# Kernel optimization log

Hardware: AMD Instinct MI355X
Metric: run time of the kernel (lower is better)

Reference implementation:

```python
import jax, jax.numpy as jnp
import numpy as np

N_SRC = 50000
N_DST = 50000
E = 800000
SRC_DIM = 128
DST_DIM = 128
OUT_DIM = 128
HEADS = 4
D_HEAD = OUT_DIM // HEADS  # 32, concat=True


def setup_inputs() -> dict:
    key = jax.random.key(0)
    ks = jax.random.split(key, 10)
    x_src = jax.random.normal(ks[0], (N_SRC, SRC_DIM), dtype=jnp.float32)
    x_dst = jax.random.normal(ks[1], (N_DST, DST_DIM), dtype=jnp.float32)
    edge_src = jax.random.randint(ks[2], (E,), 0, N_SRC)
    edge_dst = jax.random.randint(ks[3], (E,), 0, N_DST)
    # parameters (torch Linear stored as [in, out] so y = x @ W)
    W_src = jax.random.normal(ks[4], (SRC_DIM, HEADS * D_HEAD), dtype=jnp.float32) / np.sqrt(SRC_DIM)
    W_dst = jax.random.normal(ks[5], (DST_DIM, HEADS * D_HEAD), dtype=jnp.float32) / np.sqrt(DST_DIM)
    att_src = jax.random.normal(ks[6], (1, HEADS, D_HEAD), dtype=jnp.float32) * 0.01
    att_dst = jax.random.normal(ks[7], (1, HEADS, D_HEAD), dtype=jnp.float32) * 0.01
    W_self = jax.random.normal(ks[8], (DST_DIM, HEADS * D_HEAD), dtype=jnp.float32) / np.sqrt(DST_DIM)
    b_self = jax.random.normal(ks[9], (HEADS * D_HEAD,), dtype=jnp.float32) * 0.01
    return {
        "x_src": x_src, "x_dst": x_dst,
        "edge_src": edge_src, "edge_dst": edge_dst, "num_dst": N_DST,
        "W_src": W_src, "W_dst": W_dst,
        "att_src": att_src, "att_dst": att_dst,
        "W_self": W_self, "b_self": b_self,
    }


def reference(x_src, x_dst, edge_src, edge_dst, num_dst,
              W_src, W_dst, att_src, att_dst, W_self, b_self):
    H, D = HEADS, D_HEAD
    src_feat = (x_src @ W_src).reshape(-1, H, D)   # [N_src, H, D]
    dst_feat = (x_dst @ W_dst).reshape(-1, H, D)   # [N_dst, H, D]

    src_edge = src_feat[edge_src]                   # [E, H, D] gather
    dst_edge = dst_feat[edge_dst]                   # [E, H, D] gather

    alpha_src = jnp.sum(src_edge * att_src, axis=-1)  # [E, H]
    alpha_dst = jnp.sum(dst_edge * att_dst, axis=-1)  # [E, H]
    alpha = jax.nn.leaky_relu(alpha_src + alpha_dst, negative_slope=0.2)

    # segment softmax over edges grouped by destination node
    a_max = jax.ops.segment_max(alpha, edge_dst, num_segments=num_dst)  # [N_dst, H]
    alpha = jnp.exp(alpha - a_max[edge_dst])
    a_sum = jax.ops.segment_sum(alpha, edge_dst, num_segments=num_dst)  # [N_dst, H]
    alpha = alpha / (a_sum[edge_dst] + 1e-16)

    msg = (src_edge * alpha[..., None]).reshape(-1, H * D)  # [E, H*D]
    agg = jax.ops.segment_sum(msg, edge_dst, num_segments=num_dst)  # [N_dst, H*D]

    return agg + x_dst @ W_self + b_self
```

## Files before the change

### kernel.cpp

```cpp
#include <hip/hip_runtime.h>

#define N_SRC 50000
#define N_DST 50000
#define NE    800000
#define DIM   128
#define HEADS 4
#define NB_GEMM 782
#define NB_HIST 3125
#define WROWS 144

typedef short short8 __attribute__((ext_vector_type(8)));
typedef float f32x4 __attribute__((ext_vector_type(4)));

__device__ __forceinline__ float bf2f(unsigned short u) {
  union { unsigned int i; float f; } v;
  v.i = ((unsigned int)u) << 16;
  return v.f;
}

__device__ __forceinline__ unsigned short f2bf(float f) {
  unsigned int u = __float_as_uint(f);
  u += 0x7fffu + ((u >> 16) & 1u);
  return (unsigned short)(u >> 16);
}

__global__ void setup_kernel(const float* __restrict__ Wsrc, const float* __restrict__ Wself,
                             const float* __restrict__ Wdst,
                             const float* __restrict__ att_s, const float* __restrict__ att_d,
                             unsigned short* __restrict__ Wps, unsigned short* __restrict__ Wpd,
                             int* __restrict__ deg, int* __restrict__ cursor) {
  const int b = blockIdx.x, t = threadIdx.x;
  if (b == 0) {
    for (int i = t; i < DIM * DIM; i += 256) {
      int k = i >> 7, n = i & 127;
      Wps[n * DIM + k] = f2bf(Wsrc[i]);
    }
  } else if (b == 1) {
    for (int i = t; i < DIM * DIM; i += 256) {
      int k = i >> 7, n = i & 127;
      Wpd[n * DIM + k] = f2bf(Wself[i]);
    }
  } else if (b == 2) {
    for (int i = t; i < 2 * 4 * DIM; i += 256) {
      int which = (i >= 4 * DIM) ? 1 : 0;
      int j = which ? i - 4 * DIM : i;
      int h = j >> 7, k = j & 127;
      const float* W = which ? Wdst : Wsrc;
      const float* att = which ? att_d : att_s;
      float s = 0.f;
#pragma unroll 8
      for (int d = 0; d < 32; d++) s += W[k * DIM + h * 32 + d] * att[h * 32 + d];
      (which ? Wpd : Wps)[(128 + h) * DIM + k] = f2bf(s);
    }
    for (int i = t; i < 2 * 12 * DIM; i += 256) {
      int which = (i >= 12 * DIM) ? 1 : 0;
      int j = which ? i - 12 * DIM : i;
      (which ? Wpd : Wps)[132 * DIM + j] = 0;
    }
  } else {
    int i = (b - 3) * 1024 + t * 4;
    int4 z = make_int4(0, 0, 0, 0);
    if (i < N_DST) *(int4*)&deg[i] = z;
    else {
      int j = i - N_DST;
      if (j < N_DST) *(int4*)&cursor[j] = z;
    }
  }
}

__global__ __launch_bounds__(256) void phase1_kernel(
    const float* __restrict__ x_src, const float* __restrict__ x_dst,
    const unsigned short* __restrict__ Wps, const unsigned short* __restrict__ Wpd,
    const int* __restrict__ edst,
    unsigned short* __restrict__ feat, float* __restrict__ as_, float* __restrict__ ad_,
    float* __restrict__ out, const float* __restrict__ bias, int* __restrict__ deg) {
  __shared__ unsigned short lx[64 * DIM];
  __shared__ unsigned short lw[WROWS * DIM];
  const int b = blockIdx.x, t = threadIdx.x;

  if (b >= 2 * NB_GEMM) {
    int e = (b - 2 * NB_GEMM) * 256 + t;
    if (e < NE) atomicAdd(&deg[edst[e]], 1);
    return;
  }

  const bool is_dst = (b >= NB_GEMM);
  const int blk = is_dst ? b - NB_GEMM : b;
  const float* __restrict__ x = is_dst ? x_dst : x_src;
  const unsigned short* __restrict__ Wp = is_dst ? Wpd : Wps;
  const int r0 = blk * 64;

  for (int c = t; c < WROWS * 16; c += 256) {
    int row = c >> 4, slot = c & 15;
    short8 v = *(const short8*)&Wp[row * DIM + slot * 8];
    *(short8*)((char*)lw + row * 256 + ((slot ^ (row & 15)) << 4)) = v;
  }
  for (int c = t; c < 64 * 16; c += 256) {
    int row = c >> 4, slot = c & 15;
    int gr = r0 + row;
    if (gr >= N_SRC) gr = N_SRC - 1;
    const float4 va = *(const float4*)&x[gr * DIM + slot * 8];
    const float4 vb = *(const float4*)&x[gr * DIM + slot * 8 + 4];
    short8 v;
    v[0] = (short)f2bf(va.x); v[1] = (short)f2bf(va.y);
    v[2] = (short)f2bf(va.z); v[3] = (short)f2bf(va.w);
    v[4] = (short)f2bf(vb.x); v[5] = (short)f2bf(vb.y);
    v[6] = (short)f2bf(vb.z); v[7] = (short)f2bf(vb.w);
    *(short8*)((char*)lx + row * 256 + ((slot ^ (row & 15)) << 4)) = v;
  }
  __syncthreads();

  const int wave = t >> 6, lane = t & 63;
  const int rowa = lane & 15, kg = lane >> 4;
  const int xrow = wave * 16 + rowa;

  f32x4 acc[9];
#pragma unroll
  for (int n = 0; n < 9; n++) acc[n] = (f32x4){0.f, 0.f, 0.f, 0.f};

#pragma unroll
  for (int ks = 0; ks < 4; ks++) {
    const int slot = ks * 4 + kg;
    const short8 af = *(const short8*)((char*)lx + xrow * 256 + ((slot ^ rowa) << 4));
#pragma unroll
    for (int n = 0; n < 9; n++) {
      const int wr = n * 16 + rowa;
      const short8 bf = *(const short8*)((char*)lw + wr * 256 + ((slot ^ rowa) << 4));
      acc[n] = __builtin_amdgcn_mfma_f32_16x16x32_bf16(af, bf, acc[n], 0, 0, 0);
    }
  }

  const int orow0 = r0 + wave * 16 + kg * 4;
  if (!is_dst) {
#pragma unroll
    for (int n = 0; n < 8; n++) {
#pragma unroll
      for (int r = 0; r < 4; r++) {
        int row = orow0 + r;
        if (row < N_SRC) feat[row * DIM + n * 16 + rowa] = f2bf(acc[n][r]);
      }
    }
    if (rowa < HEADS) {
#pragma unroll
      for (int r = 0; r < 4; r++) {
        int row = orow0 + r;
        if (row < N_SRC) as_[row * HEADS + rowa] = acc[8][r];
      }
    }
  } else {
#pragma unroll
    for (int n = 0; n < 8; n++) {
      const float bb = bias[n * 16 + rowa];
#pragma unroll
      for (int r = 0; r < 4; r++) {
        int row = orow0 + r;
        if (row < N_DST) out[row * DIM + n * 16 + rowa] = acc[n][r] + bb;
      }
    }
    if (rowa < HEADS) {
#pragma unroll
      for (int r = 0; r < 4; r++) {
        int row = orow0 + r;
        if (row < N_DST) ad_[row * HEADS + rowa] = acc[8][r];
      }
    }
  }
}

__global__ void scan1_kernel(const int* __restrict__ deg, int* __restrict__ offs,
                             int* __restrict__ bsum, int n) {
  __shared__ int sh[256];
  int i = blockIdx.x * 256 + threadIdx.x;
  int v = (i < n) ? deg[i] : 0;
  sh[threadIdx.x] = v;
  __syncthreads();
  for (int d = 1; d < 256; d <<= 1) {
    int tv = (threadIdx.x >= d) ? sh[threadIdx.x - d] : 0;
    __syncthreads();
    sh[threadIdx.x] += tv;
    __syncthreads();
  }
  if (i < n) offs[i] = sh[threadIdx.x] - v;
  if (threadIdx.x == 255) bsum[blockIdx.x] = sh[255];
}

__global__ void scan2_kernel(int* __restrict__ bsum, int n) {
  __shared__ int sh[256];
  int v = (threadIdx.x < n) ? bsum[threadIdx.x] : 0;
  sh[threadIdx.x] = v;
  __syncthreads();
  for (int d = 1; d < 256; d <<= 1) {
    int tv = (threadIdx.x >= d) ? sh[threadIdx.x - d] : 0;
    __syncthreads();
    sh[threadIdx.x] += tv;
    __syncthreads();
  }
  if (threadIdx.x < n) bsum[threadIdx.x] = sh[threadIdx.x] - v;
}

__global__ void fill_kernel(const int* __restrict__ esrc, const int* __restrict__ edst,
                            const int* __restrict__ offs, const int* __restrict__ bsum,
                            int* __restrict__ cursor, int* __restrict__ csr_src) {
  int e = blockIdx.x * 256 + threadIdx.x;
  if (e >= NE) return;
  int s = esrc[e], d = edst[e];
  int p = atomicAdd(&cursor[d], 1);
  csr_src[offs[d] + bsum[d >> 8] + p] = s;
}

__global__ __launch_bounds__(256) void agg_kernel(
    const unsigned short* __restrict__ feat, const int* __restrict__ csr_src,
    const float* __restrict__ as_, const float* __restrict__ ad_,
    const int* __restrict__ offs, const int* __restrict__ bsum,
    const int* __restrict__ deg, float* __restrict__ out) {
  const int wave = threadIdx.x >> 6;
  const int lane = threadIdx.x & 63;
  const int n = blockIdx.x * 4 + wave;
  if (n >= N_DST) return;
  const int g = lane >> 4, q = lane & 15;
  const int h = q >> 2;
  const int beg = offs[n] + bsum[n >> 8];
  const int end = beg + deg[n];
  const float adh = ad_[n * HEADS + h];

  float4 oa, ob;
  if (g == 0) {
    oa = *(const float4*)&out[n * DIM + q * 8];
    ob = *(const float4*)&out[n * DIM + q * 8 + 4];
  }

  float s = 0.f;
  float acc[8];
#pragma unroll
  for (int j = 0; j < 8; j++) acc[j] = 0.f;

  int k = beg + g;
  int sid = 0;
  float ash = -1e30f;
  if (k < end) {
    sid = csr_src[k];
    ash = as_[sid * HEADS + h];
  }
  while (k < end) {
    const int kn = k + 4;
    int sid_n = 0;
    float ash_n = -1e30f;
    if (kn < end) {
      sid_n = csr_src[kn];
      ash_n = as_[sid_n * HEADS + h];
    }
    float al = ash + adh;
    al = al > 0.f ? al : 0.2f * al;
    const float w = __expf(al);
    const short8 f = *(const short8*)&feat[sid * DIM + q * 8];
    s += w;
#pragma unroll
    for (int j = 0; j < 8; j++) acc[j] += w * bf2f((unsigned short)f[j]);
    k = kn;
    sid = sid_n;
    ash = ash_n;
  }

  s += __shfl_xor(s, 16);
  s += __shfl_xor(s, 32);
#pragma unroll
  for (int j = 0; j < 8; j++) {
    acc[j] += __shfl_xor(acc[j], 16);
    acc[j] += __shfl_xor(acc[j], 32);
  }

  if (g == 0) {
    const float inv = 1.f / (s + 1e-16f);
    oa.x += acc[0] * inv; oa.y += acc[1] * inv;
    oa.z += acc[2] * inv; oa.w += acc[3] * inv;
    ob.x += acc[4] * inv; ob.y += acc[5] * inv;
    ob.z += acc[6] * inv; ob.w += acc[7] * inv;
    *(float4*)&out[n * DIM + q * 8] = oa;
    *(float4*)&out[n * DIM + q * 8 + 4] = ob;
  }
}

extern "C" void kernel_launch(void* const* d_in, const int* in_sizes, int n_in,
                              void* d_out, int out_size, void* d_ws, size_t ws_size,
                              hipStream_t stream) {
  const float* x_src  = (const float*)d_in[0];
  const float* x_dst  = (const float*)d_in[1];
  const int*   esrc   = (const int*)d_in[2];
  const int*   edst   = (const int*)d_in[3];
  const float* W_src  = (const float*)d_in[5];
  const float* W_dst  = (const float*)d_in[6];
  const float* att_s  = (const float*)d_in[7];
  const float* att_d  = (const float*)d_in[8];
  const float* W_self = (const float*)d_in[9];
  const float* b_self = (const float*)d_in[10];
  float* out = (float*)d_out;
  (void)in_sizes; (void)n_in; (void)out_size; (void)ws_size;

  char* ws = (char*)d_ws;
  size_t off = 0;
  auto carve = [&](size_t bytes) {
    void* p = ws + off;
    off += (bytes + 255) & ~size_t(255);
    return p;
  };
  unsigned short* feat = (unsigned short*)carve(sizeof(unsigned short) * N_SRC * DIM);
  float* as_   = (float*)carve(sizeof(float) * N_SRC * HEADS);
  float* ad_   = (float*)carve(sizeof(float) * N_DST * HEADS);
  int* deg     = (int*)carve(sizeof(int) * N_DST);
  int* cursor  = (int*)carve(sizeof(int) * N_DST);
  int* offs    = (int*)carve(sizeof(int) * N_DST);
  int* bsum    = (int*)carve(sizeof(int) * 256);
  int* csr_src = (int*)carve(sizeof(int) * NE);
  unsigned short* Wps = (unsigned short*)carve(sizeof(unsigned short) * WROWS * DIM);
  unsigned short* Wpd = (unsigned short*)carve(sizeof(unsigned short) * WROWS * DIM);

  setup_kernel<<<101, 256, 0, stream>>>(W_src, W_self, W_dst, att_s, att_d,
                                        Wps, Wpd, deg, cursor);
  phase1_kernel<<<2 * NB_GEMM + NB_HIST, 256, 0, stream>>>(
      x_src, x_dst, Wps, Wpd, edst, feat, as_, ad_, out, b_self, deg);
  const int nblk = (N_DST + 255) / 256;
  scan1_kernel<<<nblk, 256, 0, stream>>>(deg, offs, bsum, N_DST);
  scan2_kernel<<<1, 256, 0, stream>>>(bsum, nblk);
  fill_kernel<<<NB_HIST, 256, 0, stream>>>(esrc, edst, offs, bsum, cursor, csr_src);
  agg_kernel<<<(N_DST + 3) / 4, 256, 0, stream>>>(feat, csr_src, as_, ad_,
                                                  offs, bsum, deg, out);
}
```

Baseline: 264.8 us.

## Restructure CSR build pipeline and fuse fill into GEMM kernel with LDS-free tiles

The degree histogram moves into the setup kernel, and zeroing is done with a memset. The two-pass scan becomes a single pass where each block claims its base offset with an atomic counter. The CSR fill now runs inside the GEMM kernel so it overlaps the projection work. The GEMM drops its LDS staging: each wave computes two 16-row subtiles, reading x and bf16 weights straight from global memory. This cuts the launch count and the serialization between kernels, at the cost of more global and cache traffic for the weights and non-monotonic CSR segment offsets.

```diff
diff --git a/kernel.cpp b/kernel.cpp
--- a/kernel.cpp
+++ b/kernel.cpp
@@ -5,7 +5,7 @@
 #define NE    800000
 #define DIM   128
 #define HEADS 4
-#define NB_GEMM 782
+#define NB_G2   391
 #define NB_HIST 3125
 #define WROWS 144
 
@@ -27,9 +27,15 @@
 __global__ void setup_kernel(const float* __restrict__ Wsrc, const float* __restrict__ Wself,
                              const float* __restrict__ Wdst,
                              const float* __restrict__ att_s, const float* __restrict__ att_d,
+                             const int* __restrict__ edst,
                              unsigned short* __restrict__ Wps, unsigned short* __restrict__ Wpd,
-                             int* __restrict__ deg, int* __restrict__ cursor) {
+                             int* __restrict__ deg) {
   const int b = blockIdx.x, t = threadIdx.x;
+  if (b >= 3) {
+    int e = (b - 3) * 256 + t;
+    if (e < NE) atomicAdd(&deg[edst[e]], 1);
+    return;
+  }
   if (b == 0) {
     for (int i = t; i < DIM * DIM; i += 256) {
       int k = i >> 7, n = i & 127;
@@ -40,7 +46,7 @@
       int k = i >> 7, n = i & 127;
       Wpd[n * DIM + k] = f2bf(Wself[i]);
     }
-  } else if (b == 2) {
+  } else {
     for (int i = t; i < 2 * 4 * DIM; i += 256) {
       int which = (i >= 4 * DIM) ? 1 : 0;
       int j = which ? i - 4 * DIM : i;
@@ -57,119 +63,13 @@
       int j = which ? i - 12 * DIM : i;
       (which ? Wpd : Wps)[132 * DIM + j] = 0;
     }
-  } else {
-    int i = (b - 3) * 1024 + t * 4;
-    int4 z = make_int4(0, 0, 0, 0);
-    if (i < N_DST) *(int4*)&deg[i] = z;
-    else {
-      int j = i - N_DST;
-      if (j < N_DST) *(int4*)&cursor[j] = z;
-    }
-  }
-}
-
-__global__ __launch_bounds__(256) void phase1_kernel(
-    const float* __restrict__ x_src, const float* __restrict__ x_dst,
-    const unsigned short* __restrict__ Wps, const unsigned short* __restrict__ Wpd,
-    const int* __restrict__ edst,
-    unsigned short* __restrict__ feat, float* __restrict__ as_, float* __restrict__ ad_,
-    float* __restrict__ out, const float* __restrict__ bias, int* __restrict__ deg) {
-  __shared__ unsigned short lx[64 * DIM];
-  __shared__ unsigned short lw[WROWS * DIM];
-  const int b = blockIdx.x, t = threadIdx.x;
-
-  if (b >= 2 * NB_GEMM) {
-    int e = (b - 2 * NB_GEMM) * 256 + t;
-    if (e < NE) atomicAdd(&deg[edst[e]], 1);
-    return;
-  }
-
-  const bool is_dst = (b >= NB_GEMM);
-  const int blk = is_dst ? b - NB_GEMM : b;
-  const float* __restrict__ x = is_dst ? x_dst : x_src;
-  const unsigned short* __restrict__ Wp = is_dst ? Wpd : Wps;
-  const int r0 = blk * 64;
-
-  for (int c = t; c < WROWS * 16; c += 256) {
-    int row = c >> 4, slot = c & 15;
-    short8 v = *(const short8*)&Wp[row * DIM + slot * 8];
-    *(short8*)((char*)lw + row * 256 + ((slot ^ (row & 15)) << 4)) = v;
-  }
-  for (int c = t; c < 64 * 16; c += 256) {
-    int row = c >> 4, slot = c & 15;
-    int gr = r0 + row;
-    if (gr >= N_SRC) gr = N_SRC - 1;
-    const float4 va = *(const float4*)&x[gr * DIM + slot * 8];
-    const float4 vb = *(const float4*)&x[gr * DIM + slot * 8 + 4];
-    short8 v;
-    v[0] = (short)f2bf(va.x); v[1] = (short)f2bf(va.y);
-    v[2] = (short)f2bf(va.z); v[3] = (short)f2bf(va.w);
-    v[4] = (short)f2bf(vb.x); v[5] = (short)f2bf(vb.y);
-    v[6] = (short)f2bf(vb.z); v[7] = (short)f2bf(vb.w);
-    *(short8*)((char*)lx + row * 256 + ((slot ^ (row & 15)) << 4)) = v;
-  }
-  __syncthreads();
-
-  const int wave = t >> 6, lane = t & 63;
-  const int rowa = lane & 15, kg = lane >> 4;
-  const int xrow = wave * 16 + rowa;
-
-  f32x4 acc[9];
-#pragma unroll
-  for (int n = 0; n < 9; n++) acc[n] = (f32x4){0.f, 0.f, 0.f, 0.f};
-
-#pragma unroll
-  for (int ks = 0; ks < 4; ks++) {
-    const int slot = ks * 4 + kg;
-    const short8 af = *(const short8*)((char*)lx + xrow * 256 + ((slot ^ rowa) << 4));
-#pragma unroll
-    for (int n = 0; n < 9; n++) {
-      const int wr = n * 16 + rowa;
-      const short8 bf = *(const short8*)((char*)lw + wr * 256 + ((slot ^ rowa) << 4));
-      acc[n] = __builtin_amdgcn_mfma_f32_16x16x32_bf16(af, bf, acc[n], 0, 0, 0);
-    }
-  }
-
-  const int orow0 = r0 + wave * 16 + kg * 4;
-  if (!is_dst) {
-#pragma unroll
-    for (int n = 0; n < 8; n++) {
-#pragma unroll
-      for (int r = 0; r < 4; r++) {
-        int row = orow0 + r;
-        if (row < N_SRC) feat[row * DIM + n * 16 + rowa] = f2bf(acc[n][r]);
-      }
-    }
-    if (rowa < HEADS) {
-#pragma unroll
-      for (int r = 0; r < 4; r++) {
-        int row = orow0 + r;
-        if (row < N_SRC) as_[row * HEADS + rowa] = acc[8][r];
-      }
-    }
-  } else {
-#pragma unroll
-    for (int n = 0; n < 8; n++) {
-      const float bb = bias[n * 16 + rowa];
-#pragma unroll
-      for (int r = 0; r < 4; r++) {
-        int row = orow0 + r;
-        if (row < N_DST) out[row * DIM + n * 16 + rowa] = acc[n][r] + bb;
-      }
-    }
-    if (rowa < HEADS) {
-#pragma unroll
-      for (int r = 0; r < 4; r++) {
-        int row = orow0 + r;
-        if (row < N_DST) ad_[row * HEADS + rowa] = acc[8][r];
-      }
-    }
-  }
-}
-
-__global__ void scan1_kernel(const int* __restrict__ deg, int* __restrict__ offs,
-                             int* __restrict__ bsum, int n) {
+  }
+}
+
+__global__ void scan_kernel(const int* __restrict__ deg, int* __restrict__ offs,
+                            int* __restrict__ gbase, int n) {
   __shared__ int sh[256];
+  __shared__ int base_sh;
   int i = blockIdx.x * 256 + threadIdx.x;
   int v = (i < n) ? deg[i] : 0;
   sh[threadIdx.x] = v;
@@ -180,46 +80,125 @@
     sh[threadIdx.x] += tv;
     __syncthreads();
   }
-  if (i < n) offs[i] = sh[threadIdx.x] - v;
-  if (threadIdx.x == 255) bsum[blockIdx.x] = sh[255];
-}
-
-__global__ void scan2_kernel(int* __restrict__ bsum, int n) {
-  __shared__ int sh[256];
-  int v = (threadIdx.x < n) ? bsum[threadIdx.x] : 0;
-  sh[threadIdx.x] = v;
+  if (threadIdx.x == 255) base_sh = atomicAdd(gbase, sh[255]);
   __syncthreads();
-  for (int d = 1; d < 256; d <<= 1) {
-    int tv = (threadIdx.x >= d) ? sh[threadIdx.x - d] : 0;
-    __syncthreads();
-    sh[threadIdx.x] += tv;
-    __syncthreads();
-  }
-  if (threadIdx.x < n) bsum[threadIdx.x] = sh[threadIdx.x] - v;
-}
-
-__global__ void fill_kernel(const int* __restrict__ esrc, const int* __restrict__ edst,
-                            const int* __restrict__ offs, const int* __restrict__ bsum,
-                            int* __restrict__ cursor, int* __restrict__ csr_src) {
-  int e = blockIdx.x * 256 + threadIdx.x;
-  if (e >= NE) return;
-  int s = esrc[e], d = edst[e];
-  int p = atomicAdd(&cursor[d], 1);
-  csr_src[offs[d] + bsum[d >> 8] + p] = s;
+  if (i < n) offs[i] = base_sh + sh[threadIdx.x] - v;
+}
+
+__global__ __launch_bounds__(256) void phase1_kernel(
+    const float* __restrict__ x_src, const float* __restrict__ x_dst,
+    const unsigned short* __restrict__ Wps, const unsigned short* __restrict__ Wpd,
+    const int* __restrict__ esrc, const int* __restrict__ edst,
+    const int* __restrict__ offs, int* __restrict__ cursor, int* __restrict__ csr_src,
+    unsigned short* __restrict__ feat, float* __restrict__ as_, float* __restrict__ ad_,
+    float* __restrict__ out, const float* __restrict__ bias) {
+  const int b = blockIdx.x, t = threadIdx.x;
+
+  if (b >= 2 * NB_G2) {
+    int e = (b - 2 * NB_G2) * 256 + t;
+    if (e < NE) {
+      int s = esrc[e], d = edst[e];
+      int p = atomicAdd(&cursor[d], 1);
+      csr_src[offs[d] + p] = s;
+    }
+    return;
+  }
+
+  const bool is_dst = (b >= NB_G2);
+  const int blk = is_dst ? b - NB_G2 : b;
+  const float* __restrict__ x = is_dst ? x_dst : x_src;
+  const unsigned short* __restrict__ Wp = is_dst ? Wpd : Wps;
+
+  const int wave = t >> 6, lane = t & 63;
+  const int rowa = lane & 15, kg = lane >> 4;
+  const int wr0 = blk * 128 + wave * 32;
+
+  f32x4 acc[2][9];
+#pragma unroll
+  for (int s = 0; s < 2; s++)
+#pragma unroll
+    for (int n = 0; n < 9; n++) acc[s][n] = (f32x4){0.f, 0.f, 0.f, 0.f};
+
+  int ra[2];
+#pragma unroll
+  for (int s = 0; s < 2; s++) {
+    int r = wr0 + s * 16 + rowa;
+    ra[s] = (r < N_SRC) ? r : N_SRC - 1;
+  }
+
+#pragma unroll
+  for (int ks = 0; ks < 4; ks++) {
+    const int kc = ks * 32 + kg * 8;
+    short8 af[2];
+#pragma unroll
+    for (int s = 0; s < 2; s++) {
+      const float4 xa = *(const float4*)&x[ra[s] * DIM + kc];
+      const float4 xb = *(const float4*)&x[ra[s] * DIM + kc + 4];
+      af[s][0] = (short)f2bf(xa.x); af[s][1] = (short)f2bf(xa.y);
+      af[s][2] = (short)f2bf(xa.z); af[s][3] = (short)f2bf(xa.w);
+      af[s][4] = (short)f2bf(xb.x); af[s][5] = (short)f2bf(xb.y);
+      af[s][6] = (short)f2bf(xb.z); af[s][7] = (short)f2bf(xb.w);
+    }
+#pragma unroll
+    for (int n = 0; n < 9; n++) {
+      const short8 bf = *(const short8*)&Wp[(n * 16 + rowa) * DIM + kc];
+      acc[0][n] = __builtin_amdgcn_mfma_f32_16x16x32_bf16(af[0], bf, acc[0][n], 0, 0, 0);
+      acc[1][n] = __builtin_amdgcn_mfma_f32_16x16x32_bf16(af[1], bf, acc[1][n], 0, 0, 0);
+    }
+  }
+
+#pragma unroll
+  for (int s = 0; s < 2; s++) {
+    const int orow0 = wr0 + s * 16 + kg * 4;
+    if (!is_dst) {
+#pragma unroll
+      for (int n = 0; n < 8; n++) {
+#pragma unroll
+        for (int r = 0; r < 4; r++) {
+          int row = orow0 + r;
+          if (row < N_SRC) feat[row * DIM + n * 16 + rowa] = f2bf(acc[s][n][r]);
+        }
+      }
+      if (rowa < HEADS) {
+#pragma unroll
+        for (int r = 0; r < 4; r++) {
+          int row = orow0 + r;
+          if (row < N_SRC) as_[row * HEADS + rowa] = acc[s][8][r];
+        }
+      }
+    } else {
+#pragma unroll
+      for (int n = 0; n < 8; n++) {
+        const float bb = bias[n * 16 + rowa];
+#pragma unroll
+        for (int r = 0; r < 4; r++) {
+          int row = orow0 + r;
+          if (row < N_DST) out[row * DIM + n * 16 + rowa] = acc[s][n][r] + bb;
+        }
+      }
+      if (rowa < HEADS) {
+#pragma unroll
+        for (int r = 0; r < 4; r++) {
+          int row = orow0 + r;
+          if (row < N_DST) ad_[row * HEADS + rowa] = acc[s][8][r];
+        }
+      }
+    }
+  }
 }
 
 __global__ __launch_bounds__(256) void agg_kernel(
     const unsigned short* __restrict__ feat, const int* __restrict__ csr_src,
     const float* __restrict__ as_, const float* __restrict__ ad_,
-    const int* __restrict__ offs, const int* __restrict__ bsum,
-    const int* __restrict__ deg, float* __restrict__ out) {
+    const int* __restrict__ offs, const int* __restrict__ deg,
+    float* __restrict__ out) {
   const int wave = threadIdx.x >> 6;
   const int lane = threadIdx.x & 63;
   const int n = blockIdx.x * 4 + wave;
   if (n >= N_DST) return;
   const int g = lane >> 4, q = lane & 15;
   const int h = q >> 2;
-  const int beg = offs[n] + bsum[n >> 8];
+  const int beg = offs[n];
   const int end = beg + deg[n];
   const float adh = ad_[n * HEADS + h];
 
@@ -308,20 +287,20 @@
   float* ad_   = (float*)carve(sizeof(float) * N_DST * HEADS);
   int* deg     = (int*)carve(sizeof(int) * N_DST);
   int* cursor  = (int*)carve(sizeof(int) * N_DST);
+  int* gbase   = (int*)carve(sizeof(int));
   int* offs    = (int*)carve(sizeof(int) * N_DST);
-  int* bsum    = (int*)carve(sizeof(int) * 256);
   int* csr_src = (int*)carve(sizeof(int) * NE);
   unsigned short* Wps = (unsigned short*)carve(sizeof(unsigned short) * WROWS * DIM);
   unsigned short* Wpd = (unsigned short*)carve(sizeof(unsigned short) * WROWS * DIM);
 
-  setup_kernel<<<101, 256, 0, stream>>>(W_src, W_self, W_dst, att_s, att_d,
-                                        Wps, Wpd, deg, cursor);
-  phase1_kernel<<<2 * NB_GEMM + NB_HIST, 256, 0, stream>>>(
-      x_src, x_dst, Wps, Wpd, edst, feat, as_, ad_, out, b_self, deg);
-  const int nblk = (N_DST + 255) / 256;
-  scan1_kernel<<<nblk, 256, 0, stream>>>(deg, offs, bsum, N_DST);
-  scan2_kernel<<<1, 256, 0, stream>>>(bsum, nblk);
-  fill_kernel<<<NB_HIST, 256, 0, stream>>>(esrc, edst, offs, bsum, cursor, csr_src);
+  hipMemsetAsync(deg, 0, (size_t)((char*)offs - (char*)deg), stream);
+
+  setup_kernel<<<3 + NB_HIST, 256, 0, stream>>>(
+      W_src, W_self, W_dst, att_s, att_d, edst, Wps, Wpd, deg);
+  scan_kernel<<<(N_DST + 255) / 256, 256, 0, stream>>>(deg, offs, gbase, N_DST);
+  phase1_kernel<<<2 * NB_G2 + NB_HIST, 256, 0, stream>>>(
+      x_src, x_dst, Wps, Wpd, esrc, edst, offs, cursor, csr_src,
+      feat, as_, ad_, out, b_self);
   agg_kernel<<<(N_DST + 3) / 4, 256, 0, stream>>>(feat, csr_src, as_, ad_,
-                                                  offs, bsum, deg, out);
-}
+                                                  offs, deg, out);
+}
```

Result: no change. 267.4 us (+1.0%).
